# Performance work log

Hardware: AMD Instinct MI355X
Metric: run time of the kernel (lower is better)

The kernel has to match this reference:

```python
import jax, jax.numpy as jnp
import numpy as np

N_NODES = 100000
N_EDGES = 1600000
D = 64
EPS_NORM = 1e-9
EPS_DENOM = 1e-9


def setup_inputs() -> dict:
    key = jax.random.key(0)
    k1, k2, k3, k4, k5 = jax.random.split(key, 5)
    x = jax.random.normal(k1, (N_NODES, D), dtype=jnp.float32)
    z = jax.random.normal(k2, (N_NODES, D), dtype=jnp.float32)
    edge_index = jax.random.randint(k3, (2, N_EDGES), 0, N_NODES, dtype=jnp.int64)
    W = jax.random.normal(k4, (D, D), dtype=jnp.float32) * (1.0 / np.sqrt(D))
    b = jax.random.normal(k5, (D,), dtype=jnp.float32) * 0.01
    alpha = jnp.ones((), dtype=jnp.float32)
    bias_edge = jnp.zeros((), dtype=jnp.float32)
    return {"x": x, "edge_index": edge_index, "z": z, "W": W, "b": b,
            "alpha": alpha, "bias_edge": bias_edge}


def reference(x, edge_index, z, W, b, alpha, bias_edge):
    row, col = edge_index[0], edge_index[1]
    z_i = z[row]                      # [E, D] gather
    z_j = z[col]                      # [E, D] gather
    num = jnp.sum(z_i * z_j, axis=-1)                       # [E]
    den = jnp.maximum(jnp.linalg.norm(z_i, axis=-1) * jnp.linalg.norm(z_j, axis=-1), EPS_NORM)
    corr = num / den                                        # cosine correlation per edge
    logits = alpha * corr + bias_edge                       # [E]
    exp_logits = jnp.exp(logits - jnp.max(logits))          # global-max-stabilized exp
    denom = jax.ops.segment_sum(exp_logits, row, num_segments=N_NODES)  # [N]
    attn = exp_logits / (denom[row] + EPS_DENOM)            # edge softmax over incoming edges
    msgs = attn[:, None] * x[col]                           # [E, D]
    out = jax.ops.segment_sum(msgs, row, num_segments=N_NODES)          # [N, D]
    return out @ W.T + b                                    # Linear(in_dim, out_dim)
```

## Files before the change

kernel.cpp:

```cpp
#include <hip/hip_runtime.h>
#include <hip/hip_fp16.h>
#include <math.h>

#define NN 100000
#define NE 1600000
#define D  64
#define NBLK 391

typedef _Float16 half2v __attribute__((ext_vector_type(2)));

__device__ __forceinline__ unsigned int pack_entry(int col, float ex) {
    unsigned short hb = __half_as_ushort(__float2half(ex));
    return ((unsigned int)col << 15) | (unsigned int)(hb & 0x7FFFu);
}
__device__ __forceinline__ float unpack_ex(unsigned int pk) {
    return __half2float(__ushort_as_half((unsigned short)(pk & 0x7FFFu)));
}

__device__ __forceinline__ float dot2acc(int a, unsigned int b, float c) {
#if defined(__has_builtin) && __has_builtin(__builtin_amdgcn_fdot2)
    return __builtin_amdgcn_fdot2(__builtin_bit_cast(half2v, a),
                                  __builtin_bit_cast(half2v, b), c, false);
#else
    float2 fa = __half22float2(*(const __half2*)&a);
    float2 fb = __half22float2(*(const __half2*)&b);
    return fmaf(fa.y, fb.y, fmaf(fa.x, fb.x, c));
#endif
}

__global__ __launch_bounds__(256) void k_prep_count(const float* __restrict__ z,
                                                    const float* __restrict__ x,
                                                    const float* __restrict__ W,
                                                    __half* __restrict__ zx,
                                                    const int* __restrict__ ei,
                                                    int* __restrict__ cnt8,
                                                    unsigned int* __restrict__ rankr) {
    __shared__ unsigned int WtP[32 * 64];
    {
        const float2* W2 = (const float2*)W;
        for (int i = threadIdx.x; i < 2048; i += 256) {
            int j = i >> 5, d2 = i & 31;
            float2 wp = W2[j * 32 + d2];
            half2v h;
            h.x = (_Float16)wp.x;
            h.y = (_Float16)wp.y;
            WtP[d2 * 64 + j] = __builtin_bit_cast(unsigned int, h);
        }
    }
    __syncthreads();
    const int lane = threadIdx.x & 63;
    int wave = blockIdx.x * 4 + (threadIdx.x >> 6);
    int nWaves = gridDim.x * 4;
    for (int n = wave; n < NN; n += nWaves) {
        float zv = z[n * D + lane];
        float s = zv * zv;
#pragma unroll
        for (int off = 32; off; off >>= 1) s += __shfl_xor(s, off);
        float inv = 1.0f / sqrtf(fmaxf(s, 1e-18f));
        zx[(size_t)n * 128 + lane] = __float2half(zv * inv);
        float xv = x[n * D + lane];
        float pa = __shfl(xv, 2 * (lane & 31));
        float pb = __shfl(xv, 2 * (lane & 31) + 1);
        half2v pkh;
        pkh.x = (_Float16)pa;
        pkh.y = (_Float16)pb;
        int pki = __builtin_bit_cast(int, pkh);
        float y = 0.0f;
#pragma unroll
        for (int d2 = 0; d2 < 32; ++d2) {
            int pv = __shfl(pki, d2);
            unsigned int wv = WtP[d2 * 64 + lane];
            y = dot2acc(pv, wv, y);
        }
        zx[(size_t)n * 128 + 64 + lane] = __float2half(y);
    }
    const int myc = (blockIdx.x & 7) * NN;
    const unsigned int xcdbits = (unsigned int)(blockIdx.x & 7) << 12;
    int i = blockIdx.x * 256 + threadIdx.x;
    int stride = gridDim.x * 256;
    for (int e = i; e < NE; e += stride) {
        int r = __builtin_nontemporal_load(&ei[e]);
        int rk = atomicAdd(&cnt8[myc + r], 1);
        __builtin_nontemporal_store(((unsigned int)r << 15) | xcdbits | (unsigned int)rk,
                                    &rankr[e]);
    }
}

__global__ __launch_bounds__(256) void k_scan1(const int* __restrict__ cnt8,
                                               int* __restrict__ inc,
                                               int* __restrict__ bsum) {
    __shared__ int sh[256];
    int gid = blockIdx.x * 256 + threadIdx.x;
    int v = 0;
    if (gid < NN) {
#pragma unroll
        for (int k = 0; k < 8; ++k) v += cnt8[k * NN + gid];
    }
    sh[threadIdx.x] = v;
    __syncthreads();
    for (int off = 1; off < 256; off <<= 1) {
        int t = (threadIdx.x >= off) ? sh[threadIdx.x - off] : 0;
        __syncthreads();
        sh[threadIdx.x] += t;
        __syncthreads();
    }
    if (gid < NN) inc[gid] = sh[threadIdx.x];
    if (threadIdx.x == 255) bsum[blockIdx.x] = sh[255];
}

__global__ __launch_bounds__(512) void k_scan2(int* __restrict__ bsum) {
    __shared__ int sh[512];
    int v = (threadIdx.x < NBLK) ? bsum[threadIdx.x] : 0;
    sh[threadIdx.x] = v;
    __syncthreads();
    for (int off = 1; off < 512; off <<= 1) {
        int t = (threadIdx.x >= off) ? sh[threadIdx.x - off] : 0;
        __syncthreads();
        sh[threadIdx.x] += t;
        __syncthreads();
    }
    if (threadIdx.x < NBLK) bsum[threadIdx.x] = sh[threadIdx.x] - v;
}

__global__ __launch_bounds__(256) void k_scan3(const int* __restrict__ cnt8,
                                               const int* __restrict__ inc,
                                               const int* __restrict__ bsum,
                                               int* __restrict__ row_start,
                                               int* __restrict__ row_start8,
                                               int* __restrict__ tot) {
    int gid = blockIdx.x * 256 + threadIdx.x;
    if (gid >= NN) return;
    int c[8];
    int s8 = 0;
#pragma unroll
    for (int k = 0; k < 8; ++k) {
        c[k] = cnt8[k * NN + gid];
        s8 += c[k];
    }
    int ex = inc[gid] - s8 + bsum[blockIdx.x];
    row_start[gid] = ex;
    tot[gid] = s8;
    int base = ex;
#pragma unroll
    for (int k = 0; k < 8; ++k) {
        row_start8[k * NN + gid] = base;
        base += c[k];
    }
}

__global__ __launch_bounds__(256) void k_place(const int* __restrict__ ei,
                                               const unsigned int* __restrict__ rankr,
                                               const int* __restrict__ row_start8,
                                               int* __restrict__ colidx) {
    int e = blockIdx.x * 256 + threadIdx.x;
    if (e >= NE) return;
    unsigned int rr = __builtin_nontemporal_load(&rankr[e]);
    int c = __builtin_nontemporal_load(&ei[NE + e]);
    int r = (int)(rr >> 15);
    int xcd = (int)((rr >> 12) & 7u);
    int rk = (int)(rr & 0xFFFu);
    __builtin_nontemporal_store(c, &colidx[row_start8[xcd * NN + r] + rk]);
}

__global__ __launch_bounds__(256) void k_node(const __half* __restrict__ zx,
                                              const int* __restrict__ colidx,
                                              const int* __restrict__ row_start,
                                              const int* __restrict__ tot,
                                              const float* __restrict__ b,
                                              const float* __restrict__ alpha_p,
                                              const float* __restrict__ bias_p,
                                              float* __restrict__ out) {
    const int lane = threadIdx.x & 63;
    int n = (blockIdx.x * blockDim.x + threadIdx.x) >> 6;
    if (n >= NN) return;
    const float alpha = *alpha_p;
    const float bias = *bias_p;
    const float Mest = fabsf(alpha) + bias;
    int rs = row_start[n];
    int c = tot[n];
    float bv = b[lane];
    const float4* zi4 = (const float4*)(zx + (size_t)n * 128);
    float4 zi[8];
#pragma unroll
    for (int k = 0; k < 8; ++k) zi[k] = zi4[k];
    float acc = 0.0f;
    float dsum = 0.0f;
    for (int base = 0; base < c; base += 64) {
        int m = min(64, c - base);
        int idx = base + lane;
        int col = (idx < c) ? colidx[rs + idx] : 0;
        const float4* zj4 = (const float4*)(zx + (size_t)col * 128);
        float4 zj[8];
#pragma unroll
        for (int k = 0; k < 8; ++k) zj[k] = zj4[k];
        float dot = 0.0f;
#pragma unroll
        for (int k = 0; k < 8; ++k) {
            const int* ha = (const int*)&zi[k];
            const unsigned int* hb = (const unsigned int*)&zj[k];
#pragma unroll
            for (int q = 0; q < 4; ++q) dot = dot2acc(ha[q], hb[q], dot);
        }
        float ex = (idx < c) ? __expf(alpha * dot + bias - Mest) : 0.0f;
        unsigned int pk = pack_entry(col, ex);
        float t = ex;
#pragma unroll
        for (int off = 32; off; off >>= 1) t += __shfl_xor(t, off);
        dsum += t;
        int j = 0;
        for (; j + 8 <= m; j += 8) {
            unsigned int p0 = (unsigned int)__builtin_amdgcn_readlane((int)pk, j);
            unsigned int p1 = (unsigned int)__builtin_amdgcn_readlane((int)pk, j + 1);
            unsigned int p2 = (unsigned int)__builtin_amdgcn_readlane((int)pk, j + 2);
            unsigned int p3 = (unsigned int)__builtin_amdgcn_readlane((int)pk, j + 3);
            unsigned int p4 = (unsigned int)__builtin_amdgcn_readlane((int)pk, j + 4);
            unsigned int p5 = (unsigned int)__builtin_amdgcn_readlane((int)pk, j + 5);
            unsigned int p6 = (unsigned int)__builtin_amdgcn_readlane((int)pk, j + 6);
            unsigned int p7 = (unsigned int)__builtin_amdgcn_readlane((int)pk, j + 7);
            float x0 = __half2float(zx[(size_t)(p0 >> 15) * 128 + 64 + lane]);
            float x1 = __half2float(zx[(size_t)(p1 >> 15) * 128 + 64 + lane]);
            float x2 = __half2float(zx[(size_t)(p2 >> 15) * 128 + 64 + lane]);
            float x3 = __half2float(zx[(size_t)(p3 >> 15) * 128 + 64 + lane]);
            float x4 = __half2float(zx[(size_t)(p4 >> 15) * 128 + 64 + lane]);
            float x5 = __half2float(zx[(size_t)(p5 >> 15) * 128 + 64 + lane]);
            float x6 = __half2float(zx[(size_t)(p6 >> 15) * 128 + 64 + lane]);
            float x7 = __half2float(zx[(size_t)(p7 >> 15) * 128 + 64 + lane]);
            acc = fmaf(unpack_ex(p0), x0, acc);
            acc = fmaf(unpack_ex(p1), x1, acc);
            acc = fmaf(unpack_ex(p2), x2, acc);
            acc = fmaf(unpack_ex(p3), x3, acc);
            acc = fmaf(unpack_ex(p4), x4, acc);
            acc = fmaf(unpack_ex(p5), x5, acc);
            acc = fmaf(unpack_ex(p6), x6, acc);
            acc = fmaf(unpack_ex(p7), x7, acc);
        }
        for (; j < m; ++j) {
            unsigned int p0 = (unsigned int)__builtin_amdgcn_readlane((int)pk, j);
            float x0 = __half2float(zx[(size_t)(p0 >> 15) * 128 + 64 + lane]);
            acc = fmaf(unpack_ex(p0), x0, acc);
        }
    }
    out[n * D + lane] = acc / (dsum + 1e-9f) + bv;
}

extern "C" void kernel_launch(void* const* d_in, const int* in_sizes, int n_in,
                              void* d_out, int out_size, void* d_ws, size_t ws_size,
                              hipStream_t stream) {
    const float* x = (const float*)d_in[0];
    const int* ei = (const int*)d_in[1];
    const float* z = (const float*)d_in[2];
    const float* W = (const float*)d_in[3];
    const float* b = (const float*)d_in[4];
    const float* alpha = (const float*)d_in[5];
    const float* bias_edge = (const float*)d_in[6];
    float* out = (float*)d_out;

    char* ws = (char*)d_ws;
    size_t off = 0;
    __half* zx = (__half*)(ws + off); off += (size_t)NN * 128 * 2;
    int* colidx = (int*)(ws + off); off += (size_t)NE * 4;
    unsigned int* rankr = (unsigned int*)(ws + off); off += (size_t)NE * 4;
    int* cnt8 = (int*)(ws + off); off += (size_t)8 * NN * 4;
    int* row_start8 = (int*)(ws + off); off += (size_t)8 * NN * 4;
    int* inc = (int*)(ws + off); off += (size_t)NN * 4;
    int* row_start = (int*)(ws + off); off += (size_t)NN * 4;
    int* tot = (int*)(ws + off); off += (size_t)NN * 4;
    int* bsum = (int*)(ws + off); off += 512 * 4;

    hipMemsetAsync(cnt8, 0, (size_t)8 * NN * 4, stream);
    k_prep_count<<<4096, 256, 0, stream>>>(z, x, W, zx, ei, cnt8, rankr);
    k_scan1<<<NBLK, 256, 0, stream>>>(cnt8, inc, bsum);
    k_scan2<<<1, 512, 0, stream>>>(bsum);
    k_scan3<<<NBLK, 256, 0, stream>>>(cnt8, inc, bsum, row_start, row_start8, tot);
    k_place<<<(NE + 255) / 256, 256, 0, stream>>>(ei, rankr, row_start8, colidx);
    k_node<<<(NN * 64 + 255) / 256, 256, 0, stream>>>(zx, colidx, row_start, tot, b, alpha, bias_edge, out);
}
```

Baseline: 244.4 us.

## Process four nodes per wavefront with 16-lane groups in k_node

Each 64-lane wavefront now handles four nodes, and each 16-lane group scores that node's edges, instead of one node per wave scoring up to 64 edges at a time. With about 16 edges per node on average, this keeps most lanes busy during the dot-product and exp phase instead of leaving roughly three quarters idle. The aggregation phase still uses the full wave for the 64 feature lanes, reading each group's packed entries via readlane. It also splits the dot and accumulator chains to expose more ILP. Groups in the same wave must iterate to the wave's maximum degree, which adds divergence. The bounds check is removed, relying on NN being a multiple of 16.

```diff
diff --git a/kernel.cpp b/kernel.cpp
--- a/kernel.cpp
+++ b/kernel.cpp
@@ -171,8 +171,10 @@
                                               const float* __restrict__ bias_p,
                                               float* __restrict__ out) {
     const int lane = threadIdx.x & 63;
-    int n = (blockIdx.x * blockDim.x + threadIdx.x) >> 6;
-    if (n >= NN) return;
+    const int sub = lane & 15;
+    int w = (blockIdx.x * blockDim.x + threadIdx.x) >> 6;
+    int nb = w * 4;
+    int n = nb + (lane >> 4);
     const float alpha = *alpha_p;
     const float bias = *bias_p;
     const float Mest = fabsf(alpha) + bias;
@@ -183,64 +185,79 @@
     float4 zi[8];
 #pragma unroll
     for (int k = 0; k < 8; ++k) zi[k] = zi4[k];
-    float acc = 0.0f;
+    int cmax = c;
+    cmax = max(cmax, __shfl_xor(cmax, 16));
+    cmax = max(cmax, __shfl_xor(cmax, 32));
+    float a0A = 0.0f, a0B = 0.0f, a1A = 0.0f, a1B = 0.0f;
+    float a2A = 0.0f, a2B = 0.0f, a3A = 0.0f, a3B = 0.0f;
     float dsum = 0.0f;
-    for (int base = 0; base < c; base += 64) {
-        int m = min(64, c - base);
-        int idx = base + lane;
-        int col = (idx < c) ? colidx[rs + idx] : 0;
+    for (int base = 0; base < cmax; base += 16) {
+        int idx = base + sub;
+        bool valid = idx < c;
+        int col = valid ? colidx[rs + idx] : 0;
         const float4* zj4 = (const float4*)(zx + (size_t)col * 128);
         float4 zj[8];
 #pragma unroll
         for (int k = 0; k < 8; ++k) zj[k] = zj4[k];
-        float dot = 0.0f;
+        float d0 = 0.0f, d1 = 0.0f, d2 = 0.0f, d3 = 0.0f;
 #pragma unroll
         for (int k = 0; k < 8; ++k) {
             const int* ha = (const int*)&zi[k];
             const unsigned int* hb = (const unsigned int*)&zj[k];
-#pragma unroll
-            for (int q = 0; q < 4; ++q) dot = dot2acc(ha[q], hb[q], dot);
-        }
-        float ex = (idx < c) ? __expf(alpha * dot + bias - Mest) : 0.0f;
+            d0 = dot2acc(ha[0], hb[0], d0);
+            d1 = dot2acc(ha[1], hb[1], d1);
+            d2 = dot2acc(ha[2], hb[2], d2);
+            d3 = dot2acc(ha[3], hb[3], d3);
+        }
+        float dot = (d0 + d1) + (d2 + d3);
+        float ex = valid ? __expf(alpha * dot + bias - Mest) : 0.0f;
         unsigned int pk = pack_entry(col, ex);
         float t = ex;
-#pragma unroll
-        for (int off = 32; off; off >>= 1) t += __shfl_xor(t, off);
+        t += __shfl_xor(t, 1);
+        t += __shfl_xor(t, 2);
+        t += __shfl_xor(t, 4);
+        t += __shfl_xor(t, 8);
         dsum += t;
-        int j = 0;
-        for (; j + 8 <= m; j += 8) {
-            unsigned int p0 = (unsigned int)__builtin_amdgcn_readlane((int)pk, j);
-            unsigned int p1 = (unsigned int)__builtin_amdgcn_readlane((int)pk, j + 1);
-            unsigned int p2 = (unsigned int)__builtin_amdgcn_readlane((int)pk, j + 2);
-            unsigned int p3 = (unsigned int)__builtin_amdgcn_readlane((int)pk, j + 3);
-            unsigned int p4 = (unsigned int)__builtin_amdgcn_readlane((int)pk, j + 4);
-            unsigned int p5 = (unsigned int)__builtin_amdgcn_readlane((int)pk, j + 5);
-            unsigned int p6 = (unsigned int)__builtin_amdgcn_readlane((int)pk, j + 6);
-            unsigned int p7 = (unsigned int)__builtin_amdgcn_readlane((int)pk, j + 7);
-            float x0 = __half2float(zx[(size_t)(p0 >> 15) * 128 + 64 + lane]);
-            float x1 = __half2float(zx[(size_t)(p1 >> 15) * 128 + 64 + lane]);
-            float x2 = __half2float(zx[(size_t)(p2 >> 15) * 128 + 64 + lane]);
-            float x3 = __half2float(zx[(size_t)(p3 >> 15) * 128 + 64 + lane]);
-            float x4 = __half2float(zx[(size_t)(p4 >> 15) * 128 + 64 + lane]);
-            float x5 = __half2float(zx[(size_t)(p5 >> 15) * 128 + 64 + lane]);
-            float x6 = __half2float(zx[(size_t)(p6 >> 15) * 128 + 64 + lane]);
-            float x7 = __half2float(zx[(size_t)(p7 >> 15) * 128 + 64 + lane]);
-            acc = fmaf(unpack_ex(p0), x0, acc);
-            acc = fmaf(unpack_ex(p1), x1, acc);
-            acc = fmaf(unpack_ex(p2), x2, acc);
-            acc = fmaf(unpack_ex(p3), x3, acc);
-            acc = fmaf(unpack_ex(p4), x4, acc);
-            acc = fmaf(unpack_ex(p5), x5, acc);
-            acc = fmaf(unpack_ex(p6), x6, acc);
-            acc = fmaf(unpack_ex(p7), x7, acc);
-        }
-        for (; j < m; ++j) {
-            unsigned int p0 = (unsigned int)__builtin_amdgcn_readlane((int)pk, j);
-            float x0 = __half2float(zx[(size_t)(p0 >> 15) * 128 + 64 + lane]);
-            acc = fmaf(unpack_ex(p0), x0, acc);
-        }
-    }
-    out[n * D + lane] = acc / (dsum + 1e-9f) + bv;
+#define PHASE_B(GG, ACCA, ACCB)                                                                    \
+        {                                                                                          \
+            int cg = __shfl(c, GG * 16);                                                           \
+            int mg = cg - base;                                                                    \
+            mg = mg > 16 ? 16 : mg;                                                               \
+            int j = 0;                                                                             \
+            for (; j + 4 <= mg; j += 4) {                                                          \
+                unsigned int q0 = (unsigned int)__builtin_amdgcn_readlane((int)pk, GG * 16 + j);   \
+                unsigned int q1 = (unsigned int)__builtin_amdgcn_readlane((int)pk, GG * 16 + j + 1); \
+                unsigned int q2 = (unsigned int)__builtin_amdgcn_readlane((int)pk, GG * 16 + j + 2); \
+                unsigned int q3 = (unsigned int)__builtin_amdgcn_readlane((int)pk, GG * 16 + j + 3); \
+                float x0 = __half2float(zx[(size_t)(q0 >> 15) * 128 + 64 + lane]);                 \
+                float x1 = __half2float(zx[(size_t)(q1 >> 15) * 128 + 64 + lane]);                 \
+                float x2 = __half2float(zx[(size_t)(q2 >> 15) * 128 + 64 + lane]);                 \
+                float x3 = __half2float(zx[(size_t)(q3 >> 15) * 128 + 64 + lane]);                 \
+                ACCA = fmaf(unpack_ex(q0), x0, ACCA);                                              \
+                ACCB = fmaf(unpack_ex(q1), x1, ACCB);                                              \
+                ACCA = fmaf(unpack_ex(q2), x2, ACCA);                                              \
+                ACCB = fmaf(unpack_ex(q3), x3, ACCB);                                              \
+            }                                                                                      \
+            for (; j < mg; ++j) {                                                                  \
+                unsigned int q0 = (unsigned int)__builtin_amdgcn_readlane((int)pk, GG * 16 + j);   \
+                float x0 = __half2float(zx[(size_t)(q0 >> 15) * 128 + 64 + lane]);                 \
+                ACCA = fmaf(unpack_ex(q0), x0, ACCA);                                              \
+            }                                                                                      \
+        }
+        PHASE_B(0, a0A, a0B)
+        PHASE_B(1, a1A, a1B)
+        PHASE_B(2, a2A, a2B)
+        PHASE_B(3, a3A, a3B)
+#undef PHASE_B
+    }
+    float dg0 = __shfl(dsum, 0);
+    float dg1 = __shfl(dsum, 16);
+    float dg2 = __shfl(dsum, 32);
+    float dg3 = __shfl(dsum, 48);
+    out[(size_t)(nb + 0) * D + lane] = (a0A + a0B) / (dg0 + 1e-9f) + bv;
+    out[(size_t)(nb + 1) * D + lane] = (a1A + a1B) / (dg1 + 1e-9f) + bv;
+    out[(size_t)(nb + 2) * D + lane] = (a2A + a2B) / (dg2 + 1e-9f) + bv;
+    out[(size_t)(nb + 3) * D + lane] = (a3A + a3B) / (dg3 + 1e-9f) + bv;
 }
 
 extern "C" void kernel_launch(void* const* d_in, const int* in_sizes, int n_in,
@@ -273,5 +290,5 @@
     k_scan2<<<1, 512, 0, stream>>>(bsum);
     k_scan3<<<NBLK, 256, 0, stream>>>(cnt8, inc, bsum, row_start, row_start8, tot);
     k_place<<<(NE + 255) / 256, 256, 0, stream>>>(ei, rankr, row_start8, colidx);
-    k_node<<<(NN * 64 + 255) / 256, 256, 0, stream>>>(zx, colidx, row_start, tot, b, alpha, bias_edge, out);
-}
+    k_node<<<NN / 16, 256, 0, stream>>>(zx, colidx, row_start, tot, b, alpha, bias_edge, out);
+}
```

After: 229.5 us (median of 2 runs). 6.1% less time.
